# Performance work log

Hardware: AMD Instinct MI355X
Metric: run time of the kernel (lower is better)

The kernel has to match this reference:

```python
import jax, jax.numpy as jnp
import numpy as np

B, N, IN_DIM = 16, 256, 768
MEM, HID = 300, 64
NEG = -1e30
SLOPE = 0.01  # LeakyReLU negative slope


def setup_inputs() -> dict:
    key = jax.random.key(0)
    ks = jax.random.split(key, 8)
    # binary adjacency mask, float32 as in the torch module's mask_logits math
    adj = (jax.random.uniform(ks[0], (B, N, N)) < 0.3).astype(jnp.float32)
    feature = jax.random.normal(ks[1], (B, N, IN_DIM), jnp.float32)

    def lin(k, fan_in, shape):
        return (jax.random.normal(k, shape, jnp.float32) / np.sqrt(fan_in)).astype(jnp.float32)

    W0 = lin(ks[2], IN_DIM, (IN_DIM, MEM)); b0 = jnp.zeros((MEM,), jnp.float32)
    W1 = lin(ks[3], MEM, (MEM, MEM));       b1 = jnp.zeros((MEM,), jnp.float32)
    A1 = lin(ks[4], 2 * MEM, (2 * MEM, HID)); ab1 = jnp.zeros((HID,), jnp.float32)
    A2 = lin(ks[5], HID, (HID, 1));           ab2 = jnp.zeros((1,), jnp.float32)
    return dict(adj=adj, feature=feature, W0=W0, b0=b0, W1=W1, b1=b1,
                A1=A1, ab1=ab1, A2=A2, ab2=ab2)


def reference(adj, feature, W0, b0, W1, b1, A1, ab1, A2, ab2):
    Bn, Nn = adj.shape[0], adj.shape[1]
    # additive split of the concat-MLP first layer: A1 @ [h_i; h_j] = Wa@h_i + Wb@h_j
    Wa, Wb = A1[:MEM], A1[MEM:]
    a2 = A2[:, 0]
    x = feature
    for Wl, bl in ((W0, b0), (W1, b1)):  # num_layers = 2
        h = x @ Wl + bl                              # [B, N, MEM]
        si = h @ Wa                                  # [B, N, HID] (source half)
        sj = h @ Wb + ab1                            # [B, N, HID] (target half + bias)
        z = jax.nn.relu(si[:, :, None, :] + sj[:, None, :, :])  # [B, N, N, HID]
        e = jnp.einsum('bijh,h->bij', z, a2) + ab2[0]            # [B, N, N]
        e = jnp.where(e > 0, e, SLOPE * e)           # LeakyReLU(0.01)
        logits = e * adj + (1.0 - adj) * NEG         # mask_logits
        # faithful quirk: softmax over the FLATTENED N*N dimension
        att = jax.nn.softmax(logits.reshape(Bn, -1), axis=1).reshape(Bn, Nn, Nn)
        x = jnp.einsum('bij,bjd->bid', att, h)       # bmm aggregation
        # dropout is identity in eval mode
    return x
```

## Files before the change

kernel.cpp:

```cpp
#include <hip/hip_runtime.h>
#include <hip/hip_bf16.h>

static constexpr int Nc = 256;
static constexpr float NEGc = -1e30f;
static constexpr float SLOPEc = 0.01f;

using f32x4 = __attribute__((ext_vector_type(4))) float;
using s16x8 = __attribute__((ext_vector_type(8))) short;
typedef unsigned int u32;
typedef __attribute__((address_space(1))) const u32 gu32;
typedef __attribute__((address_space(3))) u32 lu32;

__device__ __forceinline__ void mfma16(f32x4& d, s16x8 a, s16x8 b) {
    asm("v_mfma_f32_16x16x32_bf16 %0, %1, %2, %0" : "+v"(d) : "v"(a), "v"(b));
}

__device__ __forceinline__ void gload16(ushort* lds, const void* g) {
    __builtin_amdgcn_global_load_lds((gu32*)(unsigned long long)g,
                                     (lu32*)(unsigned long long)lds, 16, 0, 0);
}

__device__ __forceinline__ float wredMax(float v) {
#pragma unroll
    for (int o = 32; o; o >>= 1) v = fmaxf(v, __shfl_xor(v, o, 64));
    return v;
}
__device__ __forceinline__ float wredSum(float v) {
#pragma unroll
    for (int o = 32; o; o >>= 1) v += __shfl_xor(v, o, 64);
    return v;
}

__device__ __forceinline__ unsigned packhi(unsigned u1, unsigned u0) {
    return __builtin_amdgcn_perm(u1, u0, 0x07060302u);
}

__global__ void __launch_bounds__(256) convert_all(
    const float* __restrict__ W0, const float* __restrict__ b0,
    const float* __restrict__ W1, const float* __restrict__ b1,
    const float* __restrict__ A1, const float* __restrict__ ab1,
    const float* __restrict__ feat,
    ushort* __restrict__ F0h, ushort* __restrict__ F0l,
    ushort* __restrict__ F1h, ushort* __restrict__ F1l,
    float* __restrict__ bias0, float* __restrict__ bias1,
    ushort* __restrict__ Xh, ushort* __restrict__ Xl) {
    int idx = blockIdx.x * 256 + threadIdx.x;
    if (idx >= 576896) return;

    if (idx < 43520) {
        const float* src; ushort *dh, *dl; int K, ch, c;
        if (idx < 30720) { src = W0; dh = F0h; dl = F0l; K = 768;
                           ch = idx / 320; c = idx - ch * 320; }
        else { int off = idx - 30720; src = W1; dh = F1h; dl = F1l; K = 300;
               ch = off / 320; c = off - ch * 320; }
        float v[8];
#pragma unroll
        for (int e = 0; e < 8; e++) {
            int k = ch * 8 + e;
            v[e] = (k < K && c < 300) ? src[(size_t)k * 300 + c] : 0.f;
        }
        unsigned hu[4], lu[4];
#pragma unroll
        for (int q = 0; q < 4; q++) {
            unsigned u0 = __float_as_uint(v[q * 2]);
            unsigned u1 = __float_as_uint(v[q * 2 + 1]);
            float r0 = v[q * 2] - __uint_as_float(u0 & 0xFFFF0000u);
            float r1 = v[q * 2 + 1] - __uint_as_float(u1 & 0xFFFF0000u);
            hu[q] = packhi(u1, u0);
            lu[q] = packhi(__float_as_uint(r1), __float_as_uint(r0));
        }
        size_t dst = ((size_t)ch * 448 + c) * 8;
        *(uint4*)&dh[dst] = make_uint4(hu[0], hu[1], hu[2], hu[3]);
        *(uint4*)&dl[dst] = make_uint4(lu[0], lu[1], lu[2], lu[3]);
    } else if (idx < 182784) {
        const float* Wsrc; ushort *dh, *dl; int K, idx2;
        if (idx < 141824) { idx2 = idx - 43520; Wsrc = W0; dh = F0h; dl = F0l; K = 768; }
        else { idx2 = idx - 141824; Wsrc = W1; dh = F1h; dl = F1l; K = 300; }
        int k = idx2 >> 7, c = idx2 & 127;
        float accv = 0.f;
        if (k < K) {
            const float* wrow = Wsrc + (size_t)k * 300;
            const float* a1c = (c < 64) ? (A1 + c) : (A1 + 300 * 64 + (c - 64));
            for (int mm = 0; mm < 300; mm += 4) {
                accv += wrow[mm] * a1c[(size_t)mm * 64]
                      + wrow[mm + 1] * a1c[(size_t)(mm + 1) * 64]
                      + wrow[mm + 2] * a1c[(size_t)(mm + 2) * 64]
                      + wrow[mm + 3] * a1c[(size_t)(mm + 3) * 64];
            }
        }
        unsigned u = __float_as_uint(accv);
        float r = accv - __uint_as_float(u & 0xFFFF0000u);
        size_t dst = ((size_t)(k >> 3) * 448 + 320 + c) * 8 + (k & 7);
        dh[dst] = (ushort)(u >> 16);
        dl[dst] = (ushort)(__float_as_uint(r) >> 16);
    } else if (idx < 183680) {
        int off = idx - 182784;
        int layer = off / 448, col = off - layer * 448;
        const float* b = layer ? b1 : b0;
        float v;
        if (col < 320) {
            v = (col < 300) ? b[col] : 0.f;
        } else {
            int cc = col - 320;
            const float* a1c = (cc < 64) ? (A1 + cc) : (A1 + 300 * 64 + (cc - 64));
            float s = 0.f;
            for (int mm = 0; mm < 300; mm++) s += b[mm] * a1c[(size_t)mm * 64];
            v = s + ((cc >= 64) ? ab1[cc - 64] : 0.f);
        }
        (layer ? bias1 : bias0)[col] = v;
    } else {
        int off = idx - 183680;
        int s = off / 6144, rem = off - s * 6144;
        int r = rem / 96, ch = rem - r * 96;
        const float* src = feat + ((size_t)(s * 64 + r)) * 768 + ch * 8;
        float v[8];
        *(float4*)&v[0] = *(const float4*)(src);
        *(float4*)&v[4] = *(const float4*)(src + 4);
        unsigned hu[4], lu[4];
#pragma unroll
        for (int q = 0; q < 4; q++) {
            unsigned u0 = __float_as_uint(v[q * 2]);
            unsigned u1 = __float_as_uint(v[q * 2 + 1]);
            float r0 = v[q * 2] - __uint_as_float(u0 & 0xFFFF0000u);
            float r1 = v[q * 2 + 1] - __uint_as_float(u1 & 0xFFFF0000u);
            hu[q] = packhi(u1, u0);
            lu[q] = packhi(__float_as_uint(r1), __float_as_uint(r0));
        }
        size_t dst = ((size_t)s * 96 + ch) * 512 + r * 8;
        *(uint4*)&Xh[dst] = make_uint4(hu[0], hu[1], hu[2], hu[3]);
        *(uint4*)&Xl[dst] = make_uint4(lu[0], lu[1], lu[2], lu[3]);
    }
}

__device__ __forceinline__ void gemm_core_async(
    ushort* smem,
    const char* __restrict__ AhB, const char* __restrict__ AlB,
    const char* __restrict__ BhB, const char* __restrict__ BlB,
    int WCOLS, int col0, int Kp, f32x4 (&acc)[2][2]) {
    const int tid = threadIdx.x;
    const int lane = tid & 63, wave = tid >> 6;
    const int wm = wave >> 1, wn = wave & 1;
    const int m = lane & 15, kch = lane >> 4;

    auto issue = [&](int k0, int buf) {
        size_t ao = (size_t)k0 * 128 + wave * 1024 + lane * 16;
        gload16(smem + buf * 8192 + wave * 512, AhB + ao);
        gload16(smem + buf * 8192 + 2048 + wave * 512, AlB + ao);
        size_t bo = ((size_t)((k0 >> 3) + wave) * WCOLS + col0 + lane) * 16;
        gload16(smem + buf * 8192 + 4096 + wave * 512, BhB + bo);
        gload16(smem + buf * 8192 + 6144 + wave * 512, BlB + bo);
    };

    issue(0, 0);
    __syncthreads();
    for (int k0 = 0; k0 < Kp; k0 += 32) {
        const int cur = (k0 >> 5) & 1;
        if (k0 + 32 < Kp) issue(k0 + 32, cur ^ 1);
        s16x8 Afh[2], Afl[2], Bfh[2], Bfl[2];
#pragma unroll
        for (int fr = 0; fr < 2; fr++) {
            int off = cur * 8192 + (kch * 64 + wm * 32 + fr * 16 + m) * 8;
            Afh[fr] = *(const s16x8*)&smem[off];
            Afl[fr] = *(const s16x8*)&smem[off + 2048];
        }
#pragma unroll
        for (int fc = 0; fc < 2; fc++) {
            int off = cur * 8192 + 4096 + (kch * 64 + wn * 32 + fc * 16 + m) * 8;
            Bfh[fc] = *(const s16x8*)&smem[off];
            Bfl[fc] = *(const s16x8*)&smem[off + 2048];
        }
#pragma unroll
        for (int fr = 0; fr < 2; fr++)
#pragma unroll
            for (int fc = 0; fc < 2; fc++) {
                mfma16(acc[fr][fc], Afh[fr], Bfh[fc]);
                mfma16(acc[fr][fc], Afl[fr], Bfh[fc]);
                mfma16(acc[fr][fc], Afh[fr], Bfl[fc]);
            }
        __syncthreads();
    }
}

__global__ void __launch_bounds__(256) xf_kernel(
    const ushort* __restrict__ Xh, const ushort* __restrict__ Xl, int Kp,
    const ushort* __restrict__ Fh, const ushort* __restrict__ Fl,
    const float* __restrict__ bias,
    ushort* __restrict__ Hh, ushort* __restrict__ Hl,
    float* __restrict__ si, float* __restrict__ sjT) {
    __shared__ __align__(16) ushort smem[16384];
    const int tid = threadIdx.x;
    const int lane = tid & 63, wave = tid >> 6;
    const int wm = wave >> 1, wn = wave & 1;
    const int m = lane & 15, kch = lane >> 4;
    const int row0 = blockIdx.y * 64, col0 = blockIdx.x * 64;

    f32x4 acc[2][2];
#pragma unroll
    for (int i = 0; i < 2; i++)
#pragma unroll
        for (int j = 0; j < 2; j++)
#pragma unroll
            for (int e = 0; e < 4; e++) acc[i][j][e] = 0.f;

    const size_t slabOff = (size_t)blockIdx.y * Kp * 64;
    gemm_core_async(smem, (const char*)(Xh + slabOff), (const char*)(Xl + slabOff),
                    (const char*)Fh, (const char*)Fl, 448, col0, Kp, acc);
    asm volatile("s_nop 7\ns_nop 7\ns_nop 7" ::);

#pragma unroll
    for (int fr = 0; fr < 2; fr++) {
        int rbase = row0 + wm * 32 + fr * 16 + (kch << 2);
#pragma unroll
        for (int fc = 0; fc < 2; fc++) {
            int col = col0 + wn * 32 + fc * 16 + m;
            float bv = bias[col];
            float vv[4];
#pragma unroll
            for (int e = 0; e < 4; e++) vv[e] = acc[fr][fc][e] + bv;
            if (col < 320) {
                unsigned u0 = __float_as_uint(vv[0]);
                unsigned u1 = __float_as_uint(vv[1]);
                unsigned u2 = __float_as_uint(vv[2]);
                unsigned u3 = __float_as_uint(vv[3]);
                float r0 = vv[0] - __uint_as_float(u0 & 0xFFFF0000u);
                float r1 = vv[1] - __uint_as_float(u1 & 0xFFFF0000u);
                float r2 = vv[2] - __uint_as_float(u2 & 0xFFFF0000u);
                float r3 = vv[3] - __uint_as_float(u3 & 0xFFFF0000u);
                uint2 th, tl;
                th.x = packhi(u1, u0); th.y = packhi(u3, u2);
                tl.x = packhi(__float_as_uint(r1), __float_as_uint(r0));
                tl.y = packhi(__float_as_uint(r3), __float_as_uint(r2));
                int k = rbase & 255, bb = rbase >> 8;
                size_t dst = (size_t)bb * 81920 + ((size_t)(k >> 3) * 320 + col) * 8 + (k & 7);
                *(uint2*)&Hh[dst] = th;
                *(uint2*)&Hl[dst] = tl;
            } else if (col < 384) {
                int cc = col - 320;
#pragma unroll
                for (int e = 0; e < 4; e++)
                    si[(size_t)(rbase + e) * 64 + cc] = vv[e];
            } else {
                int cc = col - 384;
                int bb = rbase >> 8, j0 = rbase & 255;
                float4 v4 = make_float4(vv[0], vv[1], vv[2], vv[3]);
                *(float4*)&sjT[((size_t)(bb * 64 + cc)) * Nc + j0] = v4;
            }
        }
    }
}

__global__ void __launch_bounds__(256) scores_kernel(
    const float* __restrict__ si, const float* __restrict__ sjT,
    const float* __restrict__ adj, const float* __restrict__ A2,
    const float* __restrict__ ab2p,
    ushort* __restrict__ Ph, ushort* __restrict__ Pl,
    float* __restrict__ rmx, float* __restrict__ rsm) {
    int b = blockIdx.x, ic = blockIdx.y;
    const int j = threadIdx.x;
    __shared__ __align__(16) float sis[8][68];
    __shared__ __align__(16) float a2s[64];
    __shared__ __align__(16) float E[8][260];

    if (j < 64) a2s[j] = A2[j];
#pragma unroll
    for (int idx = j, t = 0; t < 2; t++, idx += 256) {
        int r = idx >> 6, h = idx & 63;
        sis[r][h] = si[(size_t)(b * Nc + ic * 8 + r) * 64 + h];
    }
    float sv[64];
    const float* sjb = sjT + ((size_t)b << 6) * Nc + j;
#pragma unroll
    for (int h = 0; h < 64; h++) sv[h] = sjb[(size_t)h * Nc];
    __syncthreads();

    float acc[8] = {};
#pragma unroll
    for (int hq = 0; hq < 16; hq++) {
        float4 a2q = *(const float4*)&a2s[hq * 4];
#pragma unroll
        for (int r = 0; r < 8; r++) {
            const float4 siq = *(const float4*)&sis[r][hq * 4];
            acc[r] += a2q.x * fmaxf(siq.x + sv[hq * 4 + 0], 0.f)
                    + a2q.y * fmaxf(siq.y + sv[hq * 4 + 1], 0.f)
                    + a2q.z * fmaxf(siq.z + sv[hq * 4 + 2], 0.f)
                    + a2q.w * fmaxf(siq.w + sv[hq * 4 + 3], 0.f);
        }
    }
    float ab2v = ab2p[0];
    const float* adjp = adj + (size_t)(b * Nc + ic * 8) * Nc + j;
#pragma unroll
    for (int r = 0; r < 8; r++) {
        float e = acc[r] + ab2v;
        e = e > 0.f ? e : SLOPEc * e;
        float a = adjp[(size_t)r * Nc];
        E[r][j] = (a != 0.f) ? e : NEGc;
    }
    __syncthreads();
    int wv = j >> 6, lane = j & 63;
#pragma unroll
    for (int rr = 0; rr < 2; rr++) {
        int r = wv * 2 + rr;
        float4 q = *(const float4*)&E[r][lane * 4];
        float m4 = fmaxf(fmaxf(q.x, q.y), fmaxf(q.z, q.w));
        float rm = wredMax(m4);
        float4 p;
        p.x = expf(q.x - rm); p.y = expf(q.y - rm);
        p.z = expf(q.z - rm); p.w = expf(q.w - rm);
        float rs = wredSum(p.x + p.y + p.z + p.w);
        int gi = ic * 8 + r;
        unsigned u0 = __float_as_uint(p.x), u1 = __float_as_uint(p.y);
        unsigned u2 = __float_as_uint(p.z), u3 = __float_as_uint(p.w);
        float r0 = p.x - __uint_as_float(u0 & 0xFFFF0000u);
        float r1 = p.y - __uint_as_float(u1 & 0xFFFF0000u);
        float r2 = p.z - __uint_as_float(u2 & 0xFFFF0000u);
        float r3 = p.w - __uint_as_float(u3 & 0xFFFF0000u);
        int slab = (b << 2) + (gi >> 6);
        size_t base = (size_t)slab * 16384 + (size_t)(lane >> 1) * 512
                    + (gi & 63) * 8 + ((lane & 1) << 2);
        *(uint2*)&Ph[base] = make_uint2(packhi(u1, u0), packhi(u3, u2));
        *(uint2*)&Pl[base] = make_uint2(packhi(__float_as_uint(r1), __float_as_uint(r0)),
                                        packhi(__float_as_uint(r3), __float_as_uint(r2)));
        if (lane == 0) { rmx[b * Nc + gi] = rm; rsm[b * Nc + gi] = rs; }
    }
}

template<bool SPLIT>
__global__ void __launch_bounds__(256) pv_kernel(
    const ushort* __restrict__ Ph, const ushort* __restrict__ Pl,
    const ushort* __restrict__ Hh, const ushort* __restrict__ Hl,
    const float* __restrict__ rmx, const float* __restrict__ rsm,
    ushort* __restrict__ X1h, ushort* __restrict__ X1l,
    float* __restrict__ out, int OS) {
    __shared__ __align__(16) ushort smem[16384];
    __shared__ float sclS[256];
    __shared__ float mb[4], sb[4];
    const int tid = threadIdx.x;
    const int lane = tid & 63, wave = tid >> 6;
    const int wm = wave >> 1, wn = wave & 1;
    const int m = lane & 15, kch = lane >> 4;
    const int col0 = blockIdx.x * 64, row0 = blockIdx.y * 64;
    const int b = blockIdx.z;

    {
        float mv = rmx[b * 256 + tid];
        float wmx = wredMax(mv);
        if (!lane) mb[wave] = wmx;
        __syncthreads();
        float M = fmaxf(fmaxf(mb[0], mb[1]), fmaxf(mb[2], mb[3]));
        float ex = expf(mv - M);
        float ws = wredSum(rsm[b * 256 + tid] * ex);
        if (!lane) sb[wave] = ws;
        __syncthreads();
        float S = sb[0] + sb[1] + sb[2] + sb[3];
        sclS[tid] = ex / S;
    }

    f32x4 acc[2][2];
#pragma unroll
    for (int i = 0; i < 2; i++)
#pragma unroll
        for (int j = 0; j < 2; j++)
#pragma unroll
            for (int e = 0; e < 4; e++) acc[i][j][e] = 0.f;

    const int slab = (b << 2) + blockIdx.y;
    gemm_core_async(smem,
                    (const char*)(Ph + (size_t)slab * 16384),
                    (const char*)(Pl + (size_t)slab * 16384),
                    (const char*)(Hh + (size_t)b * 81920),
                    (const char*)(Hl + (size_t)b * 81920),
                    320, col0, 256, acc);
    asm volatile("s_nop 7\ns_nop 7\ns_nop 7" ::);

    if constexpr (SPLIT) {
        float* LF = (float*)smem;
#pragma unroll
        for (int fr = 0; fr < 2; fr++) {
            int rrel = wm * 32 + fr * 16 + (kch << 2);
#pragma unroll
            for (int fc = 0; fc < 2; fc++) {
                int crel = wn * 32 + fc * 16 + m;
#pragma unroll
                for (int e = 0; e < 4; e++)
                    LF[crel * 66 + rrel + e] = acc[fr][fc][e] * sclS[row0 + rrel + e];
            }
        }
        __syncthreads();
        for (int it = tid; it < 512; it += 256) {
            int cr = it >> 6, row = it & 63;
            float v[8];
#pragma unroll
            for (int e = 0; e < 8; e++) v[e] = LF[(cr * 8 + e) * 66 + row];
            unsigned hu[4], lu[4];
#pragma unroll
            for (int q = 0; q < 4; q++) {
                unsigned u0 = __float_as_uint(v[q * 2]);
                unsigned u1 = __float_as_uint(v[q * 2 + 1]);
                float r0 = v[q * 2] - __uint_as_float(u0 & 0xFFFF0000u);
                float r1 = v[q * 2 + 1] - __uint_as_float(u1 & 0xFFFF0000u);
                hu[q] = packhi(u1, u0);
                lu[q] = packhi(__float_as_uint(r1), __float_as_uint(r0));
            }
            size_t dst = (size_t)slab * 20480 + ((size_t)(col0 >> 3) + cr) * 512 + row * 8;
            *(uint4*)&X1h[dst] = make_uint4(hu[0], hu[1], hu[2], hu[3]);
            *(uint4*)&X1l[dst] = make_uint4(lu[0], lu[1], lu[2], lu[3]);
        }
    } else {
        float* ob = out + (size_t)b * 256 * OS;
#pragma unroll
        for (int fr = 0; fr < 2; fr++) {
            int rbase = row0 + wm * 32 + fr * 16 + (kch << 2);
#pragma unroll
            for (int fc = 0; fc < 2; fc++) {
                int col = col0 + wn * 32 + fc * 16 + m;
                if (col < OS) {
#pragma unroll
                    for (int e = 0; e < 4; e++)
                        ob[(size_t)(rbase + e) * OS + col] = acc[fr][fc][e] * sclS[rbase + e];
                }
            }
        }
    }
}

extern "C" void kernel_launch(void* const* d_in, const int* in_sizes, int n_in,
                              void* d_out, int out_size, void* d_ws, size_t ws_size,
                              hipStream_t stream) {
    const float* adj     = (const float*)d_in[0];
    const float* feature = (const float*)d_in[1];
    const float* W0      = (const float*)d_in[2];
    const float* b0      = (const float*)d_in[3];
    const float* W1      = (const float*)d_in[4];
    const float* b1      = (const float*)d_in[5];
    const float* A1      = (const float*)d_in[6];
    const float* ab1     = (const float*)d_in[7];
    const float* A2      = (const float*)d_in[8];
    const float* ab2     = (const float*)d_in[9];

    char* ws = (char*)d_ws;
    ushort* X1h   = (ushort*)(ws);
    ushort* X1l   = (ushort*)(ws + 2621440);
    float*  si    = (float*)(ws + 5242880);
    float*  sjT   = (float*)(ws + 6291456);
    ushort* Ph    = (ushort*)(ws + 7340032);
    ushort* Pl    = (ushort*)(ws + 9437184);
    float*  rmx   = (float*)(ws + 11534336);
    float*  rsm   = (float*)(ws + 11550720);
    float*  bias0 = (float*)(ws + 11567104);
    float*  bias1 = (float*)(ws + 11568896);
    ushort* F0h   = (ushort*)(ws + 11570688);
    ushort* F0l   = (ushort*)(ws + 12258816);
    ushort* F1h   = (ushort*)(ws + 12946944);
    ushort* F1l   = (ushort*)(ws + 13233664);
    ushort* Hh    = (ushort*)(ws + 13520384);
    ushort* Hl    = (ushort*)(ws + 16141824);
    ushort* Xh    = (ushort*)(ws + 18763264);
    ushort* Xl    = (ushort*)(ws + 25054720);
    float* outp   = (float*)d_out;

    convert_all<<<2254, 256, 0, stream>>>(W0, b0, W1, b1, A1, ab1, feature,
                                          F0h, F0l, F1h, F1l, bias0, bias1, Xh, Xl);

    for (int L = 0; L < 2; L++) {
        const ushort* Ah = L ? X1h : Xh;
        const ushort* Al = L ? X1l : Xl;
        const ushort* Fh = L ? F1h : F0h;
        const ushort* Fl = L ? F1l : F0l;
        const float* bf = L ? bias1 : bias0;
        int Kp = L ? 320 : 768;

        xf_kernel<<<dim3(7, 64), 256, 0, stream>>>(
            Ah, Al, Kp, Fh, Fl, bf, Hh, Hl, si, sjT);
        scores_kernel<<<dim3(16, 32), 256, 0, stream>>>(
            si, sjT, adj, A2, ab2, Ph, Pl, rmx, rsm);
        if (L == 0)
            pv_kernel<true><<<dim3(5, 4, 16), 256, 0, stream>>>(
                Ph, Pl, Hh, Hl, rmx, rsm, X1h, X1l, nullptr, 0);
        else
            pv_kernel<false><<<dim3(5, 4, 16), 256, 0, stream>>>(
                Ph, Pl, Hh, Hl, rmx, rsm, nullptr, nullptr, outp, 300);
    }
}
```

Measured before the change: 100.2 us.

## Fuse feature bf16 split into layer-0 GEMM and enlarge scores row tile

Removes the feature-conversion pass from convert_all. The layer-0 xf_kernel now loads fp32 features into registers, splits them into bf16 hi/lo and stages them into LDS inside the GEMM pipeline, which avoids writing and re-reading the converted copy. scores_kernel now handles 16 rows per block instead of 8 (half as many blocks) so the sj register loads are reused across more rows. A missing barrier after the sclS write in pv_kernel is also added. The trade-offs are more register pressure and fewer blocks for the scores kernel, plus synchronous register-staged A loads in place of async LDS loads.

Measured after the change: 119.2 us. 18.9% more time.

```diff
diff --git a/kernel.cpp b/kernel.cpp
--- a/kernel.cpp
+++ b/kernel.cpp
@@ -39,13 +39,11 @@
     const float* __restrict__ W0, const float* __restrict__ b0,
     const float* __restrict__ W1, const float* __restrict__ b1,
     const float* __restrict__ A1, const float* __restrict__ ab1,
-    const float* __restrict__ feat,
     ushort* __restrict__ F0h, ushort* __restrict__ F0l,
     ushort* __restrict__ F1h, ushort* __restrict__ F1l,
-    float* __restrict__ bias0, float* __restrict__ bias1,
-    ushort* __restrict__ Xh, ushort* __restrict__ Xl) {
+    float* __restrict__ bias0, float* __restrict__ bias1) {
     int idx = blockIdx.x * 256 + threadIdx.x;
-    if (idx >= 576896) return;
+    if (idx >= 183680) return;
 
     if (idx < 43520) {
         const float* src; ushort *dh, *dl; int K, ch, c;
@@ -93,7 +91,7 @@
         size_t dst = ((size_t)(k >> 3) * 448 + 320 + c) * 8 + (k & 7);
         dh[dst] = (ushort)(u >> 16);
         dl[dst] = (ushort)(__float_as_uint(r) >> 16);
-    } else if (idx < 183680) {
+    } else {
         int off = idx - 182784;
         int layer = off / 448, col = off - layer * 448;
         const float* b = layer ? b1 : b0;
@@ -108,32 +106,13 @@
             v = s + ((cc >= 64) ? ab1[cc - 64] : 0.f);
         }
         (layer ? bias1 : bias0)[col] = v;
-    } else {
-        int off = idx - 183680;
-        int s = off / 6144, rem = off - s * 6144;
-        int r = rem / 96, ch = rem - r * 96;
-        const float* src = feat + ((size_t)(s * 64 + r)) * 768 + ch * 8;
-        float v[8];
-        *(float4*)&v[0] = *(const float4*)(src);
-        *(float4*)&v[4] = *(const float4*)(src + 4);
-        unsigned hu[4], lu[4];
-#pragma unroll
-        for (int q = 0; q < 4; q++) {
-            unsigned u0 = __float_as_uint(v[q * 2]);
-            unsigned u1 = __float_as_uint(v[q * 2 + 1]);
-            float r0 = v[q * 2] - __uint_as_float(u0 & 0xFFFF0000u);
-            float r1 = v[q * 2 + 1] - __uint_as_float(u1 & 0xFFFF0000u);
-            hu[q] = packhi(u1, u0);
-            lu[q] = packhi(__float_as_uint(r1), __float_as_uint(r0));
-        }
-        size_t dst = ((size_t)s * 96 + ch) * 512 + r * 8;
-        *(uint4*)&Xh[dst] = make_uint4(hu[0], hu[1], hu[2], hu[3]);
-        *(uint4*)&Xl[dst] = make_uint4(lu[0], lu[1], lu[2], lu[3]);
-    }
-}
-
-__device__ __forceinline__ void gemm_core_async(
+    }
+}
+
+template<bool APRE>
+__device__ __forceinline__ void gemm_core_h(
     ushort* smem,
+    const float* __restrict__ Afp, int AS,
     const char* __restrict__ AhB, const char* __restrict__ AlB,
     const char* __restrict__ BhB, const char* __restrict__ BlB,
     int WCOLS, int col0, int Kp, f32x4 (&acc)[2][2]) {
@@ -141,21 +120,58 @@
     const int lane = tid & 63, wave = tid >> 6;
     const int wm = wave >> 1, wn = wave & 1;
     const int m = lane & 15, kch = lane >> 4;
-
-    auto issue = [&](int k0, int buf) {
+    const int arow = tid >> 2, aoff = (tid & 3) * 8;
+
+    float fa[8];
+    auto loadrgA = [&](int kk) {
+        const float* p = Afp + (size_t)arow * AS + aoff + kk;
+        *(float4*)&fa[0] = *(const float4*)(p);
+        *(float4*)&fa[4] = *(const float4*)(p + 4);
+    };
+    auto stageA = [&](int buf) {
+#pragma unroll
+        for (int q = 0; q < 2; q++) {
+            unsigned u0 = __float_as_uint(fa[q * 4 + 0]);
+            unsigned u1 = __float_as_uint(fa[q * 4 + 1]);
+            unsigned u2 = __float_as_uint(fa[q * 4 + 2]);
+            unsigned u3 = __float_as_uint(fa[q * 4 + 3]);
+            float r0 = fa[q * 4 + 0] - __uint_as_float(u0 & 0xFFFF0000u);
+            float r1 = fa[q * 4 + 1] - __uint_as_float(u1 & 0xFFFF0000u);
+            float r2 = fa[q * 4 + 2] - __uint_as_float(u2 & 0xFFFF0000u);
+            float r3 = fa[q * 4 + 3] - __uint_as_float(u3 & 0xFFFF0000u);
+            uint2 th, tl;
+            th.x = packhi(u1, u0); th.y = packhi(u3, u2);
+            tl.x = packhi(__float_as_uint(r1), __float_as_uint(r0));
+            tl.y = packhi(__float_as_uint(r3), __float_as_uint(r2));
+            int kq = aoff + q * 4;
+            int base = buf * 8192 + ((kq >> 3) * 64 + arow) * 8 + (kq & 7);
+            *(uint2*)&smem[base] = th;
+            *(uint2*)&smem[base + 2048] = tl;
+        }
+    };
+    auto issueA = [&](int k0, int buf) {
         size_t ao = (size_t)k0 * 128 + wave * 1024 + lane * 16;
         gload16(smem + buf * 8192 + wave * 512, AhB + ao);
         gload16(smem + buf * 8192 + 2048 + wave * 512, AlB + ao);
+    };
+    auto issueB = [&](int k0, int buf) {
         size_t bo = ((size_t)((k0 >> 3) + wave) * WCOLS + col0 + lane) * 16;
         gload16(smem + buf * 8192 + 4096 + wave * 512, BhB + bo);
         gload16(smem + buf * 8192 + 6144 + wave * 512, BlB + bo);
     };
 
-    issue(0, 0);
+    if constexpr (APRE) issueA(0, 0); else loadrgA(0);
+    issueB(0, 0);
+    if constexpr (!APRE) { stageA(0); if (Kp > 32) loadrgA(32); }
     __syncthreads();
+
     for (int k0 = 0; k0 < Kp; k0 += 32) {
         const int cur = (k0 >> 5) & 1;
-        if (k0 + 32 < Kp) issue(k0 + 32, cur ^ 1);
+        if (k0 + 32 < Kp) {
+            if constexpr (APRE) issueA(k0 + 32, cur ^ 1);
+            issueB(k0 + 32, cur ^ 1);
+            if constexpr (!APRE) { stageA(cur ^ 1); if (k0 + 64 < Kp) loadrgA(k0 + 64); }
+        }
         s16x8 Afh[2], Afl[2], Bfh[2], Bfl[2];
 #pragma unroll
         for (int fr = 0; fr < 2; fr++) {
@@ -181,8 +197,11 @@
     }
 }
 
+template<bool APRE>
 __global__ void __launch_bounds__(256) xf_kernel(
-    const ushort* __restrict__ Xh, const ushort* __restrict__ Xl, int Kp,
+    const float* __restrict__ Xf,
+    const ushort* __restrict__ XAh, const ushort* __restrict__ XAl,
+    int Kp,
     const ushort* __restrict__ Fh, const ushort* __restrict__ Fl,
     const float* __restrict__ bias,
     ushort* __restrict__ Hh, ushort* __restrict__ Hl,
@@ -202,9 +221,11 @@
 #pragma unroll
             for (int e = 0; e < 4; e++) acc[i][j][e] = 0.f;
 
-    const size_t slabOff = (size_t)blockIdx.y * Kp * 64;
-    gemm_core_async(smem, (const char*)(Xh + slabOff), (const char*)(Xl + slabOff),
-                    (const char*)Fh, (const char*)Fl, 448, col0, Kp, acc);
+    const float* Afp = APRE ? nullptr : (Xf + (size_t)row0 * Kp);
+    const char* AhB = APRE ? (const char*)(XAh + (size_t)blockIdx.y * Kp * 64) : nullptr;
+    const char* AlB = APRE ? (const char*)(XAl + (size_t)blockIdx.y * Kp * 64) : nullptr;
+    gemm_core_h<APRE>(smem, Afp, Kp, AhB, AlB,
+                      (const char*)Fh, (const char*)Fl, 448, col0, Kp, acc);
     asm volatile("s_nop 7\ns_nop 7\ns_nop 7" ::);
 
 #pragma unroll
@@ -257,15 +278,16 @@
     float* __restrict__ rmx, float* __restrict__ rsm) {
     int b = blockIdx.x, ic = blockIdx.y;
     const int j = threadIdx.x;
-    __shared__ __align__(16) float sis[8][68];
+    __shared__ __align__(16) float sis[16][68];
     __shared__ __align__(16) float a2s[64];
-    __shared__ __align__(16) float E[8][260];
+    __shared__ __align__(16) float E[16][260];
 
     if (j < 64) a2s[j] = A2[j];
 #pragma unroll
-    for (int idx = j, t = 0; t < 2; t++, idx += 256) {
+    for (int t = 0; t < 4; t++) {
+        int idx = j + t * 256;
         int r = idx >> 6, h = idx & 63;
-        sis[r][h] = si[(size_t)(b * Nc + ic * 8 + r) * 64 + h];
+        sis[r][h] = si[(size_t)(b * Nc + ic * 16 + r) * 64 + h];
     }
     float sv[64];
     const float* sjb = sjT + ((size_t)b << 6) * Nc + j;
@@ -273,23 +295,25 @@
     for (int h = 0; h < 64; h++) sv[h] = sjb[(size_t)h * Nc];
     __syncthreads();
 
-    float acc[8] = {};
-#pragma unroll
+    float acc[16] = {};
+#pragma unroll 4
     for (int hq = 0; hq < 16; hq++) {
         float4 a2q = *(const float4*)&a2s[hq * 4];
-#pragma unroll
-        for (int r = 0; r < 8; r++) {
+        float s0 = sv[hq * 4 + 0], s1 = sv[hq * 4 + 1];
+        float s2 = sv[hq * 4 + 2], s3 = sv[hq * 4 + 3];
+#pragma unroll
+        for (int r = 0; r < 16; r++) {
             const float4 siq = *(const float4*)&sis[r][hq * 4];
-            acc[r] += a2q.x * fmaxf(siq.x + sv[hq * 4 + 0], 0.f)
-                    + a2q.y * fmaxf(siq.y + sv[hq * 4 + 1], 0.f)
-                    + a2q.z * fmaxf(siq.z + sv[hq * 4 + 2], 0.f)
-                    + a2q.w * fmaxf(siq.w + sv[hq * 4 + 3], 0.f);
+            acc[r] += a2q.x * fmaxf(siq.x + s0, 0.f)
+                    + a2q.y * fmaxf(siq.y + s1, 0.f)
+                    + a2q.z * fmaxf(siq.z + s2, 0.f)
+                    + a2q.w * fmaxf(siq.w + s3, 0.f);
         }
     }
     float ab2v = ab2p[0];
-    const float* adjp = adj + (size_t)(b * Nc + ic * 8) * Nc + j;
-#pragma unroll
-    for (int r = 0; r < 8; r++) {
+    const float* adjp = adj + (size_t)(b * Nc + ic * 16) * Nc + j;
+#pragma unroll
+    for (int r = 0; r < 16; r++) {
         float e = acc[r] + ab2v;
         e = e > 0.f ? e : SLOPEc * e;
         float a = adjp[(size_t)r * Nc];
@@ -298,8 +322,8 @@
     __syncthreads();
     int wv = j >> 6, lane = j & 63;
 #pragma unroll
-    for (int rr = 0; rr < 2; rr++) {
-        int r = wv * 2 + rr;
+    for (int rr = 0; rr < 4; rr++) {
+        int r = wv * 4 + rr;
         float4 q = *(const float4*)&E[r][lane * 4];
         float m4 = fmaxf(fmaxf(q.x, q.y), fmaxf(q.z, q.w));
         float rm = wredMax(m4);
@@ -307,7 +331,7 @@
         p.x = expf(q.x - rm); p.y = expf(q.y - rm);
         p.z = expf(q.z - rm); p.w = expf(q.w - rm);
         float rs = wredSum(p.x + p.y + p.z + p.w);
-        int gi = ic * 8 + r;
+        int gi = ic * 16 + r;
         unsigned u0 = __float_as_uint(p.x), u1 = __float_as_uint(p.y);
         unsigned u2 = __float_as_uint(p.z), u3 = __float_as_uint(p.w);
         float r0 = p.x - __uint_as_float(u0 & 0xFFFF0000u);
@@ -353,6 +377,7 @@
         __syncthreads();
         float S = sb[0] + sb[1] + sb[2] + sb[3];
         sclS[tid] = ex / S;
+        __syncthreads();
     }
 
     f32x4 acc[2][2];
@@ -364,12 +389,12 @@
             for (int e = 0; e < 4; e++) acc[i][j][e] = 0.f;
 
     const int slab = (b << 2) + blockIdx.y;
-    gemm_core_async(smem,
-                    (const char*)(Ph + (size_t)slab * 16384),
-                    (const char*)(Pl + (size_t)slab * 16384),
-                    (const char*)(Hh + (size_t)b * 81920),
-                    (const char*)(Hl + (size_t)b * 81920),
-                    320, col0, 256, acc);
+    gemm_core_h<true>(smem, nullptr, 0,
+                      (const char*)(Ph + (size_t)slab * 16384),
+                      (const char*)(Pl + (size_t)slab * 16384),
+                      (const char*)(Hh + (size_t)b * 81920),
+                      (const char*)(Hl + (size_t)b * 81920),
+                      320, col0, 256, acc);
     asm volatile("s_nop 7\ns_nop 7\ns_nop 7" ::);
 
     if constexpr (SPLIT) {
@@ -454,30 +479,22 @@
     ushort* F1l   = (ushort*)(ws + 13233664);
     ushort* Hh    = (ushort*)(ws + 13520384);
     ushort* Hl    = (ushort*)(ws + 16141824);
-    ushort* Xh    = (ushort*)(ws + 18763264);
-    ushort* Xl    = (ushort*)(ws + 25054720);
     float* outp   = (float*)d_out;
 
-    convert_all<<<2254, 256, 0, stream>>>(W0, b0, W1, b1, A1, ab1, feature,
-                                          F0h, F0l, F1h, F1l, bias0, bias1, Xh, Xl);
-
-    for (int L = 0; L < 2; L++) {
-        const ushort* Ah = L ? X1h : Xh;
-        const ushort* Al = L ? X1l : Xl;
-        const ushort* Fh = L ? F1h : F0h;
-        const ushort* Fl = L ? F1l : F0l;
-        const float* bf = L ? bias1 : bias0;
-        int Kp = L ? 320 : 768;
-
-        xf_kernel<<<dim3(7, 64), 256, 0, stream>>>(
-            Ah, Al, Kp, Fh, Fl, bf, Hh, Hl, si, sjT);
-        scores_kernel<<<dim3(16, 32), 256, 0, stream>>>(
-            si, sjT, adj, A2, ab2, Ph, Pl, rmx, rsm);
-        if (L == 0)
-            pv_kernel<true><<<dim3(5, 4, 16), 256, 0, stream>>>(
-                Ph, Pl, Hh, Hl, rmx, rsm, X1h, X1l, nullptr, 0);
-        else
-            pv_kernel<false><<<dim3(5, 4, 16), 256, 0, stream>>>(
-                Ph, Pl, Hh, Hl, rmx, rsm, nullptr, nullptr, outp, 300);
-    }
-}
+    convert_all<<<718, 256, 0, stream>>>(W0, b0, W1, b1, A1, ab1,
+                                         F0h, F0l, F1h, F1l, bias0, bias1);
+
+    xf_kernel<false><<<dim3(7, 64), 256, 0, stream>>>(
+        feature, nullptr, nullptr, 768, F0h, F0l, bias0, Hh, Hl, si, sjT);
+    scores_kernel<<<dim3(16, 16), 256, 0, stream>>>(
+        si, sjT, adj, A2, ab2, Ph, Pl, rmx, rsm);
+    pv_kernel<true><<<dim3(5, 4, 16), 256, 0, stream>>>(
+        Ph, Pl, Hh, Hl, rmx, rsm, X1h, X1l, nullptr, 0);
+
+    xf_kernel<true><<<dim3(7, 64), 256, 0, stream>>>(
+        nullptr, X1h, X1l, 320, F1h, F1l, bias1, Hh, Hl, si, sjT);
+    scores_kernel<<<dim3(16, 16), 256, 0, stream>>>(
+        si, sjT, adj, A2, ab2, Ph, Pl, rmx, rsm);
+    pv_kernel<false><<<dim3(5, 4, 16), 256, 0, stream>>>(
+        Ph, Pl, Hh, Hl, rmx, rsm, nullptr, nullptr, outp, 300);
+}
```
